# Performance work log

Measured on AMD Instinct MI355X. Metric: run time of the kernel, lower is better.

The kernel has to match this reference:

```python
import jax, jax.numpy as jnp
import numpy as np

HIDDEN = 1024
HEADS = 16
HEAD = HIDDEN // HEADS


def setup_inputs() -> dict:
    key = jax.random.key(0)
    k1, k2, k3 = jax.random.split(key, 3)
    scale = 1.0 / np.sqrt(HIDDEN)
    return {
        "hidden_states": jax.random.normal(k1, (2, 2048, HIDDEN), dtype=jnp.float32),
        "w_qkv": jax.random.normal(k2, (HIDDEN, 3 * HIDDEN), dtype=jnp.float32) * scale,
        "b_qkv": jnp.zeros((3 * HIDDEN,), dtype=jnp.float32),
        "w_dense": jax.random.normal(k3, (HIDDEN, HIDDEN), dtype=jnp.float32) * scale,
        "b_dense": jnp.zeros((HIDDEN,), dtype=jnp.float32),
    }


def reference(hidden_states, w_qkv, b_qkv, w_dense, b_dense):
    B, S, H = hidden_states.shape
    qkv = hidden_states @ w_qkv + b_qkv                      # [B,S,3H]
    qkv = qkv.reshape(B, S, HEADS, 3 * HEAD).transpose(0, 2, 1, 3)  # [B,h,S,3d]
    q, k, v = jnp.split(qkv, 3, axis=-1)                      # each [B,h,S,d]
    scores = jnp.einsum("bhqd,bhkd->bhqk", q, k) / np.sqrt(HEAD)
    probs = jax.nn.softmax(scores, axis=-1)                   # [B,h,S,S]
    ctx = jnp.einsum("bhqk,bhkd->bhqd", probs, v)             # [B,h,S,d]
    ctx = ctx.transpose(0, 2, 1, 3).reshape(B, S, H)
    return ctx @ w_dense + b_dense
```

## Files before the change

### kernel.cpp

```cpp
#include <hip/hip_runtime.h>

#define L2E 1.44269504088896f

typedef unsigned short u16;
typedef __attribute__((ext_vector_type(8))) short bf16x8;
typedef __attribute__((ext_vector_type(4))) float f32x4;
typedef __attribute__((ext_vector_type(16))) float f32x16;

__device__ __forceinline__ u16 f2bf(float x) {
  union { float f; unsigned u; } a; a.f = x;
  return (u16)((a.u + 0x7fffu + ((a.u >> 16) & 1u)) >> 16);
}

__device__ __forceinline__ unsigned cvtpk(float lo, float hi) {
  unsigned r;
  asm("v_cvt_pk_bf16_f32 %0, %1, %2" : "=v"(r) : "v"(lo), "v"(hi));
  return r;
}

__device__ __forceinline__ float fexp2(float x) {
  float r;
  asm("v_exp_f32 %0, %1" : "=v"(r) : "v"(x));
  return r;
}

__device__ __forceinline__ void gll16(const u16* g, u16* lds) {
  __builtin_amdgcn_global_load_lds(
      (const __attribute__((address_space(1))) unsigned int*)g,
      (__attribute__((address_space(3))) unsigned int*)lds, 16, 0, 0);
}

__global__ __launch_bounds__(256) void cvt_bf16(const float* __restrict__ in,
                                                u16* __restrict__ out, int n4) {
  int i = blockIdx.x * 256 + threadIdx.x;
  int stride = gridDim.x * 256;
  for (; i < n4; i += stride) {
    float4 v = reinterpret_cast<const float4*>(in)[i];
    ushort4 o;
    o.x = f2bf(v.x); o.y = f2bf(v.y); o.z = f2bf(v.z); o.w = f2bf(v.w);
    reinterpret_cast<ushort4*>(out)[i] = o;
  }
}

__global__ __launch_bounds__(256) void transpose_cvt(const float* __restrict__ in,
                                                     u16* __restrict__ out,
                                                     int K, int N) {
  __shared__ float tile[32][33];
  int n0 = blockIdx.x * 32, k0 = blockIdx.y * 32;
  int tx = threadIdx.x & 31, ty = threadIdx.x >> 5;
  for (int r = ty; r < 32; r += 8)
    tile[r][tx] = in[(k0 + r) * N + n0 + tx];
  __syncthreads();
  for (int r = ty; r < 32; r += 8)
    out[(n0 + r) * K + k0 + tx] = f2bf(tile[tx][r]);
}

__global__ __launch_bounds__(256) void gemm_qkv(
    const u16* __restrict__ A, const u16* __restrict__ Bt,
    const float* __restrict__ bias,
    u16* __restrict__ Qo, u16* __restrict__ Ko, u16* __restrict__ Vt) {
  __shared__ __attribute__((aligned(16))) u16 As[128 * 64];
  __shared__ __attribute__((aligned(16))) u16 Bs[128 * 64];
  const int t = threadIdx.x, w = t >> 6, l = t & 63;
  const int m0 = blockIdx.y * 128, n0 = blockIdx.x * 128;
  const int lr = l & 15, lk = l >> 4;
  const int wr = (w >> 1) * 64, wc = (w & 1) * 64;
  const int sr = l >> 3;
  const int sch = (l & 7) ^ sr;
  f32x4 acc[4][4] = {};

  for (int kt = 0; kt < 16; ++kt) {
    const int k0 = kt * 64;
    __syncthreads();
#pragma unroll
    for (int j = 0; j < 4; ++j) {
      const int row = w * 32 + j * 8 + sr;
      gll16(A + (size_t)(m0 + row) * 1024 + k0 + sch * 8, &As[(w * 32 + j * 8) * 64]);
      gll16(Bt + (size_t)(n0 + row) * 1024 + k0 + sch * 8, &Bs[(w * 32 + j * 8) * 64]);
    }
    asm volatile("s_waitcnt vmcnt(0)");
    __syncthreads();
#pragma unroll
    for (int kk = 0; kk < 2; ++kk) {
      bf16x8 a[4], b[4];
#pragma unroll
      for (int mf = 0; mf < 4; ++mf) {
        const int row = wr + mf * 16 + lr;
        const int ch = (kk * 4 + lk) ^ (row & 7);
        a[mf] = *reinterpret_cast<const bf16x8*>(&As[row * 64 + ch * 8]);
      }
#pragma unroll
      for (int nf = 0; nf < 4; ++nf) {
        const int row = wc + nf * 16 + lr;
        const int ch = (kk * 4 + lk) ^ (row & 7);
        b[nf] = *reinterpret_cast<const bf16x8*>(&Bs[row * 64 + ch * 8]);
      }
#pragma unroll
      for (int mf = 0; mf < 4; ++mf)
#pragma unroll
        for (int nf = 0; nf < 4; ++nf)
          acc[mf][nf] = __builtin_amdgcn_mfma_f32_16x16x32_bf16(a[mf], b[nf],
                                                                acc[mf][nf], 0, 0, 0);
    }
  }
  const float QSC = 0.125f * L2E;
#pragma unroll
  for (int mf = 0; mf < 4; ++mf)
#pragma unroll
    for (int nf = 0; nf < 4; ++nf) {
      const int gc = n0 + wc + nf * 16 + lr;
      const int h = gc / 192, j = gc - h * 192;
      const int part = j >> 6, d = j & 63;
      const float bv = bias[gc];
      const int gr0 = m0 + wr + mf * 16 + lk * 4;
      const int b_ = gr0 >> 11, s0 = gr0 & 2047;
      if (part == 2) {
        union { ushort4 s; unsigned u[2]; } pk;
        pk.u[0] = cvtpk(acc[mf][nf][0] + bv, acc[mf][nf][1] + bv);
        pk.u[1] = cvtpk(acc[mf][nf][2] + bv, acc[mf][nf][3] + bv);
        *reinterpret_cast<ushort4*>(
            &Vt[((size_t)(b_ * 16 + h) * 64 + d) * 2048 + s0]) = pk.s;
      } else if (part == 0) {
#pragma unroll
        for (int r = 0; r < 4; ++r)
          Qo[((size_t)(b_ * 16 + h) * 2048 + s0 + r) * 64 + d] =
              f2bf((acc[mf][nf][r] + bv) * QSC);
      } else {
#pragma unroll
        for (int r = 0; r < 4; ++r)
          Ko[((size_t)(b_ * 16 + h) * 2048 + s0 + r) * 64 + d] =
              f2bf(acc[mf][nf][r] + bv);
      }
    }
}

__global__ __launch_bounds__(256) void attn2(
    const u16* __restrict__ Q, const u16* __restrict__ K,
    const u16* __restrict__ Vt, u16* __restrict__ ctx) {
  __shared__ __attribute__((aligned(16))) u16 Ks[2][64 * 64];
  __shared__ __attribute__((aligned(16))) u16 Vs[2][64 * 64];
  const int t = threadIdx.x;
  const int w = t >> 6, l = t & 63;
  const int lq = l & 31, hi = l >> 5;
  const int bid = blockIdx.x;
  const int wg = (bid & 7) * 64 + (bid >> 3);
  const int bh = wg >> 4, qt = wg & 15;
  const int b = bh >> 4, h = bh & 15;
  const u16* Qp = Q + (size_t)bh * (2048 * 64);
  const u16* Kp = K + (size_t)bh * (2048 * 64);
  const u16* Vp = Vt + (size_t)bh * (64 * 2048);
  const int q0w = qt * 128 + w * 32;

  const int srow = w * 16 + (l >> 3);
  const int sch = (l & 7) ^ ((l >> 3) & 7);

  bf16x8 qf[4];
#pragma unroll
  for (int i = 0; i < 4; ++i)
    qf[i] = *reinterpret_cast<const bf16x8*>(
        &Qp[(size_t)(q0w + lq) * 64 + i * 16 + hi * 8]);

  bf16x8 ones;
#pragma unroll
  for (int j = 0; j < 8; ++j) ones[j] = (short)0x3F80;

  f32x16 o0 = {}, o1 = {}, osum = {};
  float mrun = -1e30f;

#define STG(bufi, kk0)                                                         \
  do {                                                                         \
    gll16(Kp + (size_t)((kk0) + srow) * 64 + sch * 8,                          \
          &Ks[bufi][(w * 16) * 64]);                                           \
    gll16(Kp + (size_t)((kk0) + srow + 8) * 64 + sch * 8,                      \
          &Ks[bufi][(w * 16 + 8) * 64]);                                       \
    gll16(Vp + (size_t)srow * 2048 + (kk0) + sch * 8,                          \
          &Vs[bufi][(w * 16) * 64]);                                           \
    gll16(Vp + (size_t)(srow + 8) * 2048 + (kk0) + sch * 8,                    \
          &Vs[bufi][(w * 16 + 8) * 64]);                                       \
  } while (0)

#define PVSTEP(pp, sub)                                                        \
  do {                                                                         \
    _Pragma("unroll")                                                          \
    for (int kb = 0; kb < 2; ++kb) {                                           \
      unsigned W0 = cvtpk(pp[8 * kb + 0], pp[8 * kb + 1]);                     \
      unsigned W1 = cvtpk(pp[8 * kb + 2], pp[8 * kb + 3]);                     \
      unsigned W2 = cvtpk(pp[8 * kb + 4], pp[8 * kb + 5]);                     \
      unsigned W3 = cvtpk(pp[8 * kb + 6], pp[8 * kb + 7]);                     \
      unsigned X0 = (unsigned)__shfl_xor((int)W0, 32);                         \
      unsigned X1 = (unsigned)__shfl_xor((int)W1, 32);                         \
      unsigned X2 = (unsigned)__shfl_xor((int)W2, 32);                         \
      unsigned X3 = (unsigned)__shfl_xor((int)W3, 32);                         \
      union { unsigned u[4]; bf16x8 v; } pu;                                   \
      pu.u[0] = hi ? X2 : W0;                                                  \
      pu.u[1] = hi ? X3 : W1;                                                  \
      pu.u[2] = hi ? W2 : X0;                                                  \
      pu.u[3] = hi ? W3 : X1;                                                  \
      const int ch = (((sub) * 4 + kb * 2 + hi) ^ (lq & 7)) * 8;               \
      bf16x8 v0 = *reinterpret_cast<const bf16x8*>(&VB[lq * 64 + ch]);         \
      o0 = __builtin_amdgcn_mfma_f32_32x32x16_bf16(v0, pu.v, o0, 0, 0, 0);     \
      bf16x8 v1 = *reinterpret_cast<const bf16x8*>(&VB[(32 + lq) * 64 + ch]);  \
      o1 = __builtin_amdgcn_mfma_f32_32x32x16_bf16(v1, pu.v, o1, 0, 0, 0);     \
      osum = __builtin_amdgcn_mfma_f32_32x32x16_bf16(ones, pu.v, osum, 0, 0, 0);\
    }                                                                          \
  } while (0)

  STG(0, 0);
  asm volatile("s_waitcnt vmcnt(0)");
  __syncthreads();

#pragma unroll 2
  for (int kt = 0; kt < 32; ++kt) {
    const int buf = kt & 1;
    if (kt < 31) { STG(buf ^ 1, (kt + 1) * 64); }
    const u16* KB = Ks[buf];
    const u16* VB = Vs[buf];

    f32x16 s0 = {}, s1 = {};
#pragma unroll
    for (int i = 0; i < 4; ++i) {
      const int sl = ((2 * i + hi) ^ (lq & 7)) * 8;
      bf16x8 k0f = *reinterpret_cast<const bf16x8*>(&KB[lq * 64 + sl]);
      s0 = __builtin_amdgcn_mfma_f32_32x32x16_bf16(k0f, qf[i], s0, 0, 0, 0);
      bf16x8 k1f = *reinterpret_cast<const bf16x8*>(&KB[(32 + lq) * 64 + sl]);
      s1 = __builtin_amdgcn_mfma_f32_32x32x16_bf16(k1f, qf[i], s1, 0, 0, 0);
    }

    float mx[8];
#pragma unroll
    for (int r = 0; r < 8; ++r)
      mx[r] = fmaxf(fmaxf(s0[r], s0[r + 8]), fmaxf(s1[r], s1[r + 8]));
#pragma unroll
    for (int r = 0; r < 4; ++r) mx[r] = fmaxf(mx[r], mx[r + 4]);
    float tm = fmaxf(fmaxf(mx[0], mx[1]), fmaxf(mx[2], mx[3]));
    tm = fmaxf(tm, __shfl_xor(tm, 32));

    if (!__all(tm - mrun <= 8.0f)) {
      float mnew = fmaxf(mrun, tm);
      float al = fexp2(mrun - mnew);
      mrun = mnew;
#pragma unroll
      for (int r = 0; r < 16; ++r) { o0[r] *= al; o1[r] *= al; }
      osum[0] *= al;
    }

    float p0[16], p1[16];
#pragma unroll
    for (int r = 0; r < 16; ++r) p0[r] = fexp2(s0[r] - mrun);
#pragma unroll
    for (int r = 0; r < 16; ++r) p1[r] = fexp2(s1[r] - mrun);

    PVSTEP(p0, 0);
    PVSTEP(p1, 1);

    asm volatile("s_waitcnt vmcnt(0)");
    __syncthreads();
  }
#undef STG
#undef PVSTEP

  const float inv = 1.0f / osum[0];
  u16* cp = ctx + ((size_t)(b * 2048 + q0w + lq) * 1024 + h * 64);
#pragma unroll
  for (int a = 0; a < 4; ++a) {
    const int d = 8 * a + 4 * hi;
    union { ushort4 s; unsigned u[2]; } pk;
    pk.u[0] = cvtpk(o0[4 * a + 0] * inv, o0[4 * a + 1] * inv);
    pk.u[1] = cvtpk(o0[4 * a + 2] * inv, o0[4 * a + 3] * inv);
    *reinterpret_cast<ushort4*>(cp + d) = pk.s;
    pk.u[0] = cvtpk(o1[4 * a + 0] * inv, o1[4 * a + 1] * inv);
    pk.u[1] = cvtpk(o1[4 * a + 2] * inv, o1[4 * a + 3] * inv);
    *reinterpret_cast<ushort4*>(cp + 32 + d) = pk.s;
  }
}

__global__ __launch_bounds__(256) void gemm_dense(
    const u16* __restrict__ A, const u16* __restrict__ Bt,
    const float* __restrict__ bias, float* __restrict__ out) {
  __shared__ __attribute__((aligned(16))) u16 As[128 * 64];
  __shared__ __attribute__((aligned(16))) u16 Bs[128 * 64];
  const int t = threadIdx.x, w = t >> 6, l = t & 63;
  const int m0 = blockIdx.y * 128, n0 = blockIdx.x * 128;
  const int lr = l & 15, lk = l >> 4;
  const int wr = (w >> 1) * 64, wc = (w & 1) * 64;
  const int sr = l >> 3;
  const int sch = (l & 7) ^ sr;
  f32x4 acc[4][4] = {};

  for (int kt = 0; kt < 16; ++kt) {
    const int k0 = kt * 64;
    __syncthreads();
#pragma unroll
    for (int j = 0; j < 4; ++j) {
      const int row = w * 32 + j * 8 + sr;
      gll16(A + (size_t)(m0 + row) * 1024 + k0 + sch * 8, &As[(w * 32 + j * 8) * 64]);
      gll16(Bt + (size_t)(n0 + row) * 1024 + k0 + sch * 8, &Bs[(w * 32 + j * 8) * 64]);
    }
    asm volatile("s_waitcnt vmcnt(0)");
    __syncthreads();
#pragma unroll
    for (int kk = 0; kk < 2; ++kk) {
      bf16x8 a[4], b[4];
#pragma unroll
      for (int mf = 0; mf < 4; ++mf) {
        const int row = wr + mf * 16 + lr;
        const int ch = (kk * 4 + lk) ^ (row & 7);
        a[mf] = *reinterpret_cast<const bf16x8*>(&As[row * 64 + ch * 8]);
      }
#pragma unroll
      for (int nf = 0; nf < 4; ++nf) {
        const int row = wc + nf * 16 + lr;
        const int ch = (kk * 4 + lk) ^ (row & 7);
        b[nf] = *reinterpret_cast<const bf16x8*>(&Bs[row * 64 + ch * 8]);
      }
#pragma unroll
      for (int mf = 0; mf < 4; ++mf)
#pragma unroll
        for (int nf = 0; nf < 4; ++nf)
          acc[mf][nf] = __builtin_amdgcn_mfma_f32_16x16x32_bf16(a[mf], b[nf],
                                                                acc[mf][nf], 0, 0, 0);
    }
  }
#pragma unroll
  for (int mf = 0; mf < 4; ++mf)
#pragma unroll
    for (int nf = 0; nf < 4; ++nf)
#pragma unroll
      for (int r = 0; r < 4; ++r) {
        int gr = m0 + wr + mf * 16 + lk * 4 + r;
        int gc = n0 + wc + nf * 16 + lr;
        out[(size_t)gr * 1024 + gc] = acc[mf][nf][r] + bias[gc];
      }
}

extern "C" void kernel_launch(void* const* d_in, const int* in_sizes, int n_in,
                              void* d_out, int out_size, void* d_ws, size_t ws_size,
                              hipStream_t stream) {
  const float* hs = (const float*)d_in[0];
  const float* w_qkv = (const float*)d_in[1];
  const float* b_qkv = (const float*)d_in[2];
  const float* w_dense = (const float*)d_in[3];
  const float* b_dense = (const float*)d_in[4];
  float* out = (float*)d_out;

  char* ws = (char*)d_ws;
  u16* hsb = (u16*)(ws);
  u16* wqkvT = (u16*)(ws + (8ll << 20));
  u16* wdT = (u16*)(ws + (14ll << 20));
  u16* Qb = (u16*)(ws + (16ll << 20));
  u16* Kb = (u16*)(ws + (24ll << 20));
  u16* Vtb = (u16*)(ws + (32ll << 20));
  u16* ctx = (u16*)(ws + (40ll << 20));

  cvt_bf16<<<dim3(2048), dim3(256), 0, stream>>>(hs, hsb, (4096 * 1024) / 4);
  transpose_cvt<<<dim3(96, 32), dim3(256), 0, stream>>>(w_qkv, wqkvT, 1024, 3072);
  transpose_cvt<<<dim3(32, 32), dim3(256), 0, stream>>>(w_dense, wdT, 1024, 1024);
  gemm_qkv<<<dim3(24, 32), dim3(256), 0, stream>>>(hsb, wqkvT, b_qkv, Qb, Kb, Vtb);
  attn2<<<dim3(512), dim3(256), 0, stream>>>(Qb, Kb, Vtb, ctx);
  gemm_dense<<<dim3(8, 32), dim3(256), 0, stream>>>(ctx, wdT, b_dense, out);
}
```

Before: 213.7 us.

## Double-buffer GEMM loads and relax attention waits; halve dense GEMM N-tile

Both GEMMs now use double-buffered LDS tiles, issuing the next K-tile's global-to-LDS loads before computing the current one and waiting with partial vmcnt counts instead of draining everything. The attention loop drops its full vmcnt(0) drain and waits only for the current stage's loads before a raw barrier. The dense GEMM's N-tile shrinks from 128 to 64, doubling its grid from 256 to 512 blocks so more CUs are busy. The aim is to hide global-load latency behind MFMA work. The cost is double the LDS per GEMM block, which may lower occupancy, and a correctness risk from the hand-written vmcnt counts.

Result: faster. 203.6 us (-4.8%).

```diff
diff --git a/kernel.cpp b/kernel.cpp
--- a/kernel.cpp
+++ b/kernel.cpp
@@ -59,8 +59,8 @@
     const u16* __restrict__ A, const u16* __restrict__ Bt,
     const float* __restrict__ bias,
     u16* __restrict__ Qo, u16* __restrict__ Ko, u16* __restrict__ Vt) {
-  __shared__ __attribute__((aligned(16))) u16 As[128 * 64];
-  __shared__ __attribute__((aligned(16))) u16 Bs[128 * 64];
+  __shared__ __attribute__((aligned(16))) u16 As[2][128 * 64];
+  __shared__ __attribute__((aligned(16))) u16 Bs[2][128 * 64];
   const int t = threadIdx.x, w = t >> 6, l = t & 63;
   const int m0 = blockIdx.y * 128, n0 = blockIdx.x * 128;
   const int lr = l & 15, lk = l >> 4;
@@ -69,17 +69,30 @@
   const int sch = (l & 7) ^ sr;
   f32x4 acc[4][4] = {};
 
+#define QSTAGE(bi, k0)                                                        \
+  do {                                                                        \
+    _Pragma("unroll")                                                         \
+    for (int j = 0; j < 4; ++j) {                                             \
+      const int rb = w * 32 + j * 8;                                          \
+      gll16(A + (size_t)(m0 + rb + sr) * 1024 + (k0) + sch * 8,               \
+            &As[bi][rb * 64]);                                                \
+      gll16(Bt + (size_t)(n0 + rb + sr) * 1024 + (k0) + sch * 8,              \
+            &Bs[bi][rb * 64]);                                                \
+    }                                                                         \
+  } while (0)
+
+  QSTAGE(0, 0);
   for (int kt = 0; kt < 16; ++kt) {
-    const int k0 = kt * 64;
-    __syncthreads();
-#pragma unroll
-    for (int j = 0; j < 4; ++j) {
-      const int row = w * 32 + j * 8 + sr;
-      gll16(A + (size_t)(m0 + row) * 1024 + k0 + sch * 8, &As[(w * 32 + j * 8) * 64]);
-      gll16(Bt + (size_t)(n0 + row) * 1024 + k0 + sch * 8, &Bs[(w * 32 + j * 8) * 64]);
-    }
-    asm volatile("s_waitcnt vmcnt(0)");
-    __syncthreads();
+    const int buf = kt & 1;
+    if (kt < 15) {
+      QSTAGE(buf ^ 1, (kt + 1) * 64);
+      asm volatile("s_waitcnt vmcnt(8)" ::: "memory");
+    } else {
+      asm volatile("s_waitcnt vmcnt(0)" ::: "memory");
+    }
+    __builtin_amdgcn_s_barrier();
+    const u16* Asb = As[buf];
+    const u16* Bsb = Bs[buf];
 #pragma unroll
     for (int kk = 0; kk < 2; ++kk) {
       bf16x8 a[4], b[4];
@@ -87,13 +100,13 @@
       for (int mf = 0; mf < 4; ++mf) {
         const int row = wr + mf * 16 + lr;
         const int ch = (kk * 4 + lk) ^ (row & 7);
-        a[mf] = *reinterpret_cast<const bf16x8*>(&As[row * 64 + ch * 8]);
+        a[mf] = *reinterpret_cast<const bf16x8*>(&Asb[row * 64 + ch * 8]);
       }
 #pragma unroll
       for (int nf = 0; nf < 4; ++nf) {
         const int row = wc + nf * 16 + lr;
         const int ch = (kk * 4 + lk) ^ (row & 7);
-        b[nf] = *reinterpret_cast<const bf16x8*>(&Bs[row * 64 + ch * 8]);
+        b[nf] = *reinterpret_cast<const bf16x8*>(&Bsb[row * 64 + ch * 8]);
       }
 #pragma unroll
       for (int mf = 0; mf < 4; ++mf)
@@ -102,7 +115,11 @@
           acc[mf][nf] = __builtin_amdgcn_mfma_f32_16x16x32_bf16(a[mf], b[nf],
                                                                 acc[mf][nf], 0, 0, 0);
     }
+    asm volatile("" ::: "memory");
+    __builtin_amdgcn_s_barrier();
   }
+#undef QSTAGE
+
   const float QSC = 0.125f * L2E;
 #pragma unroll
   for (int mf = 0; mf < 4; ++mf)
@@ -206,13 +223,17 @@
   } while (0)
 
   STG(0, 0);
-  asm volatile("s_waitcnt vmcnt(0)");
-  __syncthreads();
 
 #pragma unroll 2
   for (int kt = 0; kt < 32; ++kt) {
     const int buf = kt & 1;
-    if (kt < 31) { STG(buf ^ 1, (kt + 1) * 64); }
+    if (kt < 31) {
+      STG(buf ^ 1, (kt + 1) * 64);
+      asm volatile("s_waitcnt vmcnt(4)" ::: "memory");
+    } else {
+      asm volatile("s_waitcnt vmcnt(0)" ::: "memory");
+    }
+    __builtin_amdgcn_s_barrier();
     const u16* KB = Ks[buf];
     const u16* VB = Vs[buf];
 
@@ -253,8 +274,8 @@
     PVSTEP(p0, 0);
     PVSTEP(p1, 1);
 
-    asm volatile("s_waitcnt vmcnt(0)");
-    __syncthreads();
+    asm volatile("" ::: "memory");
+    __builtin_amdgcn_s_barrier();
   }
 #undef STG
 #undef PVSTEP
@@ -277,54 +298,75 @@
 __global__ __launch_bounds__(256) void gemm_dense(
     const u16* __restrict__ A, const u16* __restrict__ Bt,
     const float* __restrict__ bias, float* __restrict__ out) {
-  __shared__ __attribute__((aligned(16))) u16 As[128 * 64];
-  __shared__ __attribute__((aligned(16))) u16 Bs[128 * 64];
+  __shared__ __attribute__((aligned(16))) u16 As[2][128 * 64];
+  __shared__ __attribute__((aligned(16))) u16 Bs[2][64 * 64];
   const int t = threadIdx.x, w = t >> 6, l = t & 63;
-  const int m0 = blockIdx.y * 128, n0 = blockIdx.x * 128;
+  const int m0 = blockIdx.y * 128, n0 = blockIdx.x * 64;
   const int lr = l & 15, lk = l >> 4;
-  const int wr = (w >> 1) * 64, wc = (w & 1) * 64;
+  const int wr = (w >> 1) * 64, wc = (w & 1) * 32;
   const int sr = l >> 3;
   const int sch = (l & 7) ^ sr;
-  f32x4 acc[4][4] = {};
-
+  f32x4 acc[4][2] = {};
+
+#define DSTAGE(bi, k0)                                                        \
+  do {                                                                        \
+    _Pragma("unroll")                                                         \
+    for (int j = 0; j < 4; ++j) {                                             \
+      const int rb = w * 32 + j * 8;                                          \
+      gll16(A + (size_t)(m0 + rb + sr) * 1024 + (k0) + sch * 8,               \
+            &As[bi][rb * 64]);                                                \
+    }                                                                         \
+    _Pragma("unroll")                                                         \
+    for (int j = 0; j < 2; ++j) {                                             \
+      const int rb = w * 16 + j * 8;                                          \
+      gll16(Bt + (size_t)(n0 + rb + sr) * 1024 + (k0) + sch * 8,              \
+            &Bs[bi][rb * 64]);                                                \
+    }                                                                         \
+  } while (0)
+
+  DSTAGE(0, 0);
   for (int kt = 0; kt < 16; ++kt) {
-    const int k0 = kt * 64;
-    __syncthreads();
-#pragma unroll
-    for (int j = 0; j < 4; ++j) {
-      const int row = w * 32 + j * 8 + sr;
-      gll16(A + (size_t)(m0 + row) * 1024 + k0 + sch * 8, &As[(w * 32 + j * 8) * 64]);
-      gll16(Bt + (size_t)(n0 + row) * 1024 + k0 + sch * 8, &Bs[(w * 32 + j * 8) * 64]);
-    }
-    asm volatile("s_waitcnt vmcnt(0)");
-    __syncthreads();
+    const int buf = kt & 1;
+    if (kt < 15) {
+      DSTAGE(buf ^ 1, (kt + 1) * 64);
+      asm volatile("s_waitcnt vmcnt(6)" ::: "memory");
+    } else {
+      asm volatile("s_waitcnt vmcnt(0)" ::: "memory");
+    }
+    __builtin_amdgcn_s_barrier();
+    const u16* Asb = As[buf];
+    const u16* Bsb = Bs[buf];
 #pragma unroll
     for (int kk = 0; kk < 2; ++kk) {
-      bf16x8 a[4], b[4];
+      bf16x8 a[4], b[2];
 #pragma unroll
       for (int mf = 0; mf < 4; ++mf) {
         const int row = wr + mf * 16 + lr;
         const int ch = (kk * 4 + lk) ^ (row & 7);
-        a[mf] = *reinterpret_cast<const bf16x8*>(&As[row * 64 + ch * 8]);
-      }
-#pragma unroll
-      for (int nf = 0; nf < 4; ++nf) {
+        a[mf] = *reinterpret_cast<const bf16x8*>(&Asb[row * 64 + ch * 8]);
+      }
+#pragma unroll
+      for (int nf = 0; nf < 2; ++nf) {
         const int row = wc + nf * 16 + lr;
         const int ch = (kk * 4 + lk) ^ (row & 7);
-        b[nf] = *reinterpret_cast<const bf16x8*>(&Bs[row * 64 + ch * 8]);
+        b[nf] = *reinterpret_cast<const bf16x8*>(&Bsb[row * 64 + ch * 8]);
       }
 #pragma unroll
       for (int mf = 0; mf < 4; ++mf)
 #pragma unroll
-        for (int nf = 0; nf < 4; ++nf)
+        for (int nf = 0; nf < 2; ++nf)
           acc[mf][nf] = __builtin_amdgcn_mfma_f32_16x16x32_bf16(a[mf], b[nf],
                                                                 acc[mf][nf], 0, 0, 0);
     }
+    asm volatile("" ::: "memory");
+    __builtin_amdgcn_s_barrier();
   }
+#undef DSTAGE
+
 #pragma unroll
   for (int mf = 0; mf < 4; ++mf)
 #pragma unroll
-    for (int nf = 0; nf < 4; ++nf)
+    for (int nf = 0; nf < 2; ++nf)
 #pragma unroll
       for (int r = 0; r < 4; ++r) {
         int gr = m0 + wr + mf * 16 + lk * 4 + r;
@@ -357,5 +399,5 @@
   transpose_cvt<<<dim3(32, 32), dim3(256), 0, stream>>>(w_dense, wdT, 1024, 1024);
   gemm_qkv<<<dim3(24, 32), dim3(256), 0, stream>>>(hsb, wqkvT, b_qkv, Qb, Kb, Vtb);
   attn2<<<dim3(512), dim3(256), 0, stream>>>(Qb, Kb, Vtb, ctx);
-  gemm_dense<<<dim3(8, 32), dim3(256), 0, stream>>>(ctx, wdT, b_dense, out);
-}
+  gemm_dense<<<dim3(16, 32), dim3(256), 0, stream>>>(ctx, wdT, b_dense, out);
+}
```
